# Kernel optimization log

Hardware: AMD Instinct MI355X
Metric: run time of the kernel (lower is better)

Reference implementation:

```python
import jax, jax.numpy as jnp
import numpy as np

B, S, D, H = 2, 2048, 1024, 16
DK = D // H  # 64


def setup_inputs() -> dict:
    key = jax.random.key(0)
    ks = jax.random.split(key, 11)
    scale = 1.0 / np.sqrt(D)
    inp = {
        "x": jax.random.normal(ks[0], (B, S, D), dtype=jnp.float32),
        "z": jax.random.normal(ks[1], (B, S, D), dtype=jnp.float32),
        # causal mask, broadcast over batch and heads; masked_fill where mask==0
        "mask": jnp.tril(jnp.ones((1, 1, S, S), dtype=jnp.int32)),
        "wq_w": jax.random.normal(ks[2], (D, D), dtype=jnp.float32) * scale,
        "wq_b": jax.random.normal(ks[3], (D,), dtype=jnp.float32) * 0.01,
        "wk_w": jax.random.normal(ks[4], (D, D), dtype=jnp.float32) * scale,
        "wk_b": jax.random.normal(ks[5], (D,), dtype=jnp.float32) * 0.01,
        "wv_w": jax.random.normal(ks[6], (D, D), dtype=jnp.float32) * scale,
        "wv_b": jax.random.normal(ks[7], (D,), dtype=jnp.float32) * 0.01,
        "wo_w": jax.random.normal(ks[8], (D, D), dtype=jnp.float32) * scale,
        "wo_b": jax.random.normal(ks[9], (D,), dtype=jnp.float32) * 0.01,
    }
    return inp


def reference(x, z, mask, wq_w, wq_b, wk_w, wk_b, wv_w, wv_b, wo_w, wo_b):
    # torch Linear: y = x @ W.T + b
    q = x @ wq_w.T + wq_b
    k = z @ wk_w.T + wk_b
    # NOTE: faithful to source bug: value uses wk, not wv (wv is a dead param)
    v = z @ wk_w.T + wk_b

    def split_heads(t):  # [B,S,D] -> [B,H,S,DK]
        return t.reshape(B, S, H, DK).transpose(0, 2, 1, 3)

    q, k, v = split_heads(q), split_heads(k), split_heads(v)

    scores = jnp.einsum("bhqd,bhkd->bhqk", q, k) * (DK ** -0.5)
    scores = jnp.where(mask == 0, -jnp.inf, scores)
    attn_weights = jax.nn.softmax(scores, axis=-1)  # [B,H,S,S]
    atn = jnp.einsum("bhqk,bhkd->bhqd", attn_weights, v)

    concat = atn.transpose(0, 2, 1, 3).reshape(B, S, D)
    output = concat @ wo_w.T + wo_b  # dropout rate 0.0 -> identity
    concat_attn_weight = attn_weights.sum(axis=1)  # [B,S,S]
    return output, concat_attn_weight
```

## Files before the change

### kernel.cpp

```cpp
#include <hip/hip_runtime.h>

typedef __bf16 bf16_t;
typedef __bf16 bf16x4 __attribute__((ext_vector_type(4)));
typedef __bf16 bf16x8 __attribute__((ext_vector_type(8)));
typedef float  f32x4  __attribute__((ext_vector_type(4)));

#define MFMA(a, b, c) __builtin_amdgcn_mfma_f32_16x16x32_bf16((a), (b), (c), 0, 0, 0)

static constexpr int Bsz = 2, S = 2048, D = 1024, H = 16, DK = 64;
#define QSCALE 0.18033688011112042f

__device__ __forceinline__ void gl16(const bf16_t* g, bf16_t* l)
{
    __builtin_amdgcn_global_load_lds(
        (const __attribute__((address_space(1))) void*)g,
        (__attribute__((address_space(3))) void*)l, 16, 0, 0);
}

__global__ __launch_bounds__(256) void cvt5(
    const float* __restrict__ x, const float* __restrict__ z,
    const float* __restrict__ wq, const float* __restrict__ wk,
    const float* __restrict__ wo,
    bf16_t* __restrict__ xb, bf16_t* __restrict__ zb,
    bf16_t* __restrict__ wqb, bf16_t* __restrict__ wkb, bf16_t* __restrict__ wob)
{
    constexpr int NXZ = Bsz * S * D / 4;
    constexpr int NW  = D * D / 4;
    int i = blockIdx.x * 256 + threadIdx.x;
    const float* s; bf16_t* d; int off;
    if (i < NXZ)                 { s = x;  d = xb;  off = i; }
    else if (i < 2 * NXZ)        { s = z;  d = zb;  off = i - NXZ; }
    else if (i < 2 * NXZ + NW)   { s = wq; d = wqb; off = i - 2 * NXZ; }
    else if (i < 2 * NXZ + 2*NW) { s = wk; d = wkb; off = i - 2 * NXZ - NW; }
    else                         { s = wo; d = wob; off = i - 2 * NXZ - 2 * NW; }
    float4 v = *(const float4*)&s[(size_t)off * 4];
    bf16x4 o;
    o[0] = (bf16_t)v.x; o[1] = (bf16_t)v.y; o[2] = (bf16_t)v.z; o[3] = (bf16_t)v.w;
    *(bf16x4*)&d[(size_t)off * 4] = o;
}

__global__ __launch_bounds__(512) void gemm_qk(
    const bf16_t* __restrict__ xA, const bf16_t* __restrict__ wqB,
    const float* __restrict__ wqb, bf16_t* __restrict__ Qc,
    const bf16_t* __restrict__ zA, const bf16_t* __restrict__ wkB,
    const float* __restrict__ wkb, bf16_t* __restrict__ Kc,
    bf16_t* __restrict__ KTout)
{
    constexpr int N = D, K = D;
    const int zi = blockIdx.z;
    const bf16_t* A    = zi ? zA  : xA;
    const bf16_t* B    = zi ? wkB : wqB;
    const float*  bias = zi ? wkb : wqb;
    bf16_t*       C    = zi ? Kc  : Qc;
    const float   sc   = zi ? 1.f : QSCALE;

    __shared__ bf16_t As[2][128][32];
    __shared__ bf16_t Bs[2][128][32];

    const int t    = threadIdx.x;
    const int wave = t >> 6, lane = t & 63;
    const int quad = lane >> 4, l15 = lane & 15;
    const int wm = (wave >> 1) * 32, wn = (wave & 1) * 64;
    const int rowbase = blockIdx.y * 128, colbase = blockIdx.x * 128;
    const int srow = wave * 16 + (lane >> 2);
    const int scol = (lane & 3) << 3;

    f32x4 acc[2][4];
#pragma unroll
    for (int i = 0; i < 2; ++i)
#pragma unroll
        for (int j = 0; j < 4; ++j) acc[i][j] = {0.f, 0.f, 0.f, 0.f};

    gl16(&A[(size_t)(rowbase + srow) * K + scol], &As[0][srow][scol]);
    gl16(&B[(size_t)(colbase + srow) * K + scol], &Bs[0][srow][scol]);
    __syncthreads();

    for (int kt = 0; kt < K; kt += 32) {
        const int cur = (kt >> 5) & 1, nxt = cur ^ 1;
        const bool more = (kt + 32) < K;
        if (more) {
            gl16(&A[(size_t)(rowbase + srow) * K + kt + 32 + scol], &As[nxt][srow][scol]);
            gl16(&B[(size_t)(colbase + srow) * K + kt + 32 + scol], &Bs[nxt][srow][scol]);
        }

        bf16x8 af[2], bfr[4];
#pragma unroll
        for (int mt = 0; mt < 2; ++mt)
            af[mt] = *(const bf16x8*)&As[cur][wm + mt * 16 + l15][quad * 8];
#pragma unroll
        for (int nt = 0; nt < 4; ++nt)
            bfr[nt] = *(const bf16x8*)&Bs[cur][wn + nt * 16 + l15][quad * 8];
#pragma unroll
        for (int mt = 0; mt < 2; ++mt)
#pragma unroll
            for (int nt = 0; nt < 4; ++nt)
                acc[mt][nt] = MFMA(af[mt], bfr[nt], acc[mt][nt]);

        __syncthreads();
    }

#pragma unroll
    for (int nt = 0; nt < 4; ++nt) {
        int col  = colbase + wn + nt * 16 + l15;
        float bv = bias[col];
#pragma unroll
        for (int mt = 0; mt < 2; ++mt) {
            int row0 = rowbase + wm + mt * 16 + quad * 4;
#pragma unroll
            for (int rr = 0; rr < 4; ++rr) {
                float v = (acc[mt][nt][rr] + bv) * sc;
                C[(size_t)(row0 + rr) * N + col] = (bf16_t)v;
                if (zi) {
                    int row = row0 + rr;
                    int bb = row >> 11, srw = row & (S - 1);
                    int hh = col >> 6,  dd  = col & 63;
                    KTout[(((size_t)bb * H + hh) * DK + dd) * S + srw] = (bf16_t)v;
                }
            }
        }
    }
}

__global__ __launch_bounds__(256) void gemm_obt(
    const bf16_t* __restrict__ A, const bf16_t* __restrict__ B,
    const float* __restrict__ bias, float* __restrict__ C)
{
    constexpr int N = D, K = D;
    __shared__ bf16_t As[2][64][32];
    __shared__ bf16_t Bs[2][128][32];

    const int t    = threadIdx.x;
    const int wave = t >> 6, lane = t & 63;
    const int quad = lane >> 4, l15 = lane & 15;
    const int wm = (wave >> 1) * 32, wn = (wave & 1) * 64;
    const int rowbase = blockIdx.y * 64, colbase = blockIdx.x * 128;
    const int srow = wave * 16 + (lane >> 2);
    const int scol = (lane & 3) << 3;

    f32x4 acc[2][4];
#pragma unroll
    for (int i = 0; i < 2; ++i)
#pragma unroll
        for (int j = 0; j < 4; ++j) acc[i][j] = {0.f, 0.f, 0.f, 0.f};

    gl16(&A[(size_t)(rowbase + srow) * K + scol],      &As[0][srow][scol]);
    gl16(&B[(size_t)(colbase + srow) * K + scol],      &Bs[0][srow][scol]);
    gl16(&B[(size_t)(colbase + 64 + srow) * K + scol], &Bs[0][64 + srow][scol]);
    __syncthreads();

    for (int kt = 0; kt < K; kt += 32) {
        const int cur = (kt >> 5) & 1, nxt = cur ^ 1;
        const bool more = (kt + 32) < K;
        if (more) {
            gl16(&A[(size_t)(rowbase + srow) * K + kt + 32 + scol],      &As[nxt][srow][scol]);
            gl16(&B[(size_t)(colbase + srow) * K + kt + 32 + scol],      &Bs[nxt][srow][scol]);
            gl16(&B[(size_t)(colbase + 64 + srow) * K + kt + 32 + scol], &Bs[nxt][64 + srow][scol]);
        }

        bf16x8 af[2], bfr[4];
#pragma unroll
        for (int mt = 0; mt < 2; ++mt)
            af[mt] = *(const bf16x8*)&As[cur][wm + mt * 16 + l15][quad * 8];
#pragma unroll
        for (int nt = 0; nt < 4; ++nt)
            bfr[nt] = *(const bf16x8*)&Bs[cur][wn + nt * 16 + l15][quad * 8];
#pragma unroll
        for (int mt = 0; mt < 2; ++mt)
#pragma unroll
            for (int nt = 0; nt < 4; ++nt)
                acc[mt][nt] = MFMA(af[mt], bfr[nt], acc[mt][nt]);

        __syncthreads();
    }

#pragma unroll
    for (int nt = 0; nt < 4; ++nt) {
        int col  = colbase + wn + nt * 16 + l15;
        float bv = bias[col];
#pragma unroll
        for (int mt = 0; mt < 2; ++mt) {
            int row0 = rowbase + wm + mt * 16 + quad * 4;
#pragma unroll
            for (int rr = 0; rr < 4; ++rr)
                C[(size_t)(row0 + rr) * N + col] = acc[mt][nt][rr] + bv;
        }
    }
}

__global__ __launch_bounds__(256) void attn_flash(
    const bf16_t* __restrict__ Q, const bf16_t* __restrict__ Km,
    const bf16_t* __restrict__ KT,
    bf16_t* __restrict__ Oc, float* __restrict__ m_ws, float* __restrict__ il_ws)
{
    const int h = blockIdx.y, b = blockIdx.z;
    const int t = threadIdx.x;
    const int wave = t >> 6, lane = t & 63;
    const int quad = lane >> 4, l15 = lane & 15;

    __shared__ bf16_t Ks[2][64][72];
    __shared__ bf16_t KTs[2][64][72];
    __shared__ bf16_t PQ[64][72];

    const int hcol = h * DK;
    const bf16_t* KTh = KT + ((size_t)(b * H + h)) * DK * S;
    const size_t bS = (size_t)b * S;

    const int jr = (t >> 3);
    const int ce = (t & 7) * 8;
    const int iloc = wave * 16 + l15;

    for (int half = 0; half < 2; ++half) {
        const int qt = half == 0 ? (int)blockIdx.x : 31 - (int)blockIdx.x;
        const size_t qrow0 = bS + (size_t)qt * 64;

        __syncthreads();
        bf16x8 qld[2], kreg[2], ktreg[2];
#pragma unroll
        for (int p = 0; p < 2; ++p) {
            qld[p]   = *(const bf16x8*)&Q[(qrow0 + p * 32 + jr) * D + hcol + ce];
            kreg[p]  = *(const bf16x8*)&Km[(bS + p * 32 + jr) * D + hcol + ce];
            ktreg[p] = *(const bf16x8*)&KTh[(size_t)(p * 32 + jr) * S + ce];
        }
#pragma unroll
        for (int p = 0; p < 2; ++p) {
            *(bf16x8*)&PQ[p * 32 + jr][ce]     = qld[p];
            *(bf16x8*)&Ks[0][p * 32 + jr][ce]  = kreg[p];
            *(bf16x8*)&KTs[0][p * 32 + jr][ce] = ktreg[p];
        }
        __syncthreads();
        const bf16x8 qf0 = *(const bf16x8*)&PQ[wave * 16 + l15][quad * 8];
        const bf16x8 qf1 = *(const bf16x8*)&PQ[wave * 16 + l15][32 + quad * 8];

        f32x4 accO[4];
#pragma unroll
        for (int u = 0; u < 4; ++u) accO[u] = {0.f, 0.f, 0.f, 0.f};
        float m_cur = -1e30f, l_cur = 0.f;

        auto softmax_pv = [&](f32x4 sv[4], int cur) {
            float tm = sv[0][0];
#pragma unroll
            for (int nt = 0; nt < 4; ++nt)
#pragma unroll
                for (int r = 0; r < 4; ++r) tm = fmaxf(tm, sv[nt][r]);
            tm = fmaxf(tm, __shfl_xor(tm, 16));
            tm = fmaxf(tm, __shfl_xor(tm, 32));
            if (__any(tm > m_cur + 8.f)) {
                float m_new = fmaxf(m_cur, tm);
                float alpha = exp2f(m_cur - m_new);
                m_cur = m_new;
                l_cur *= alpha;
                float alpha4[4];
#pragma unroll
                for (int r = 0; r < 4; ++r)
                    alpha4[r] = __shfl(alpha, (quad << 4) + quad * 4 + r, 64);
#pragma unroll
                for (int u = 0; u < 4; ++u)
#pragma unroll
                    for (int r = 0; r < 4; ++r) accO[u][r] *= alpha4[r];
            }
            float rs = 0.f;
#pragma unroll
            for (int nt = 0; nt < 4; ++nt)
#pragma unroll
                for (int r = 0; r < 4; ++r) {
                    float p = exp2f(sv[nt][r] - m_cur);
                    sv[nt][r] = p;
                    rs += p;
                }
            rs += __shfl_xor(rs, 16);
            rs += __shfl_xor(rs, 32);
            l_cur += rs;

#pragma unroll
            for (int nt = 0; nt < 4; ++nt) {
                bf16x4 pk;
                pk[0] = (bf16_t)sv[nt][0]; pk[1] = (bf16_t)sv[nt][1];
                pk[2] = (bf16_t)sv[nt][2]; pk[3] = (bf16_t)sv[nt][3];
                *(bf16x4*)&PQ[wave * 16 + l15][nt * 16 + quad * 4] = pk;
            }
            asm volatile("s_waitcnt lgkmcnt(0)" ::: "memory");

            bf16x8 pa0 = *(const bf16x8*)&PQ[wave * 16 + l15][quad * 8];
            bf16x8 pa1 = *(const bf16x8*)&PQ[wave * 16 + l15][32 + quad * 8];
            __builtin_amdgcn_s_setprio(1);
#pragma unroll
            for (int u = 0; u < 4; ++u) {
                bf16x8 v0 = *(const bf16x8*)&KTs[cur][u * 16 + l15][quad * 8];
                bf16x8 v1 = *(const bf16x8*)&KTs[cur][u * 16 + l15][32 + quad * 8];
                accO[u] = MFMA(pa0, v0, accO[u]);
                accO[u] = MFMA(pa1, v1, accO[u]);
            }
            __builtin_amdgcn_s_setprio(0);
        };

        for (int jt = 0; jt < qt; ++jt) {
            const int cur = jt & 1, nxt = cur ^ 1;
#pragma unroll
            for (int p = 0; p < 2; ++p) {
                kreg[p]  = *(const bf16x8*)&Km[(bS + (size_t)(jt + 1) * 64 + p * 32 + jr) * D + hcol + ce];
                ktreg[p] = *(const bf16x8*)&KTh[(size_t)(p * 32 + jr) * S + (size_t)(jt + 1) * 64 + ce];
            }

            f32x4 sv[4];
            __builtin_amdgcn_s_setprio(1);
#pragma unroll
            for (int nt = 0; nt < 4; ++nt) {
                bf16x8 a0 = *(const bf16x8*)&Ks[cur][nt * 16 + l15][quad * 8];
                bf16x8 a1 = *(const bf16x8*)&Ks[cur][nt * 16 + l15][32 + quad * 8];
                f32x4 a = {0.f, 0.f, 0.f, 0.f};
                a = MFMA(a0, qf0, a);
                a = MFMA(a1, qf1, a);
                sv[nt] = a;
            }
            __builtin_amdgcn_s_setprio(0);
            softmax_pv(sv, cur);

#pragma unroll
            for (int p = 0; p < 2; ++p) {
                *(bf16x8*)&Ks[nxt][p * 32 + jr][ce]  = kreg[p];
                *(bf16x8*)&KTs[nxt][p * 32 + jr][ce] = ktreg[p];
            }
            __syncthreads();
        }

        {
            const int cur = qt & 1;
            f32x4 sv[4];
            __builtin_amdgcn_s_setprio(1);
#pragma unroll
            for (int nt = 0; nt < 4; ++nt) {
                bf16x8 a0 = *(const bf16x8*)&Ks[cur][nt * 16 + l15][quad * 8];
                bf16x8 a1 = *(const bf16x8*)&Ks[cur][nt * 16 + l15][32 + quad * 8];
                f32x4 a = {0.f, 0.f, 0.f, 0.f};
                a = MFMA(a0, qf0, a);
                a = MFMA(a1, qf1, a);
#pragma unroll
                for (int r = 0; r < 4; ++r)
                    if ((nt * 16 + quad * 4 + r) > iloc) a[r] = -1e30f;
                sv[nt] = a;
            }
            __builtin_amdgcn_s_setprio(0);
            softmax_pv(sv, cur);
        }

        float invl = 1.f / l_cur;
        float invl4[4];
#pragma unroll
        for (int r = 0; r < 4; ++r)
            invl4[r] = __shfl(invl, (quad << 4) + quad * 4 + r, 64);
#pragma unroll
        for (int u = 0; u < 4; ++u)
#pragma unroll
            for (int r = 0; r < 4; ++r)
                Oc[(qrow0 + wave * 16 + quad * 4 + r) * D + hcol + u * 16 + l15] =
                    (bf16_t)(accO[u][r] * invl4[r]);

        if (quad == 0) {
            size_t sb = ((size_t)(b * H + h)) * S + (size_t)qt * 64 + wave * 16 + l15;
            m_ws[sb]  = m_cur;
            il_ws[sb] = invl;
        }
    }
}

__global__ __launch_bounds__(256) void attn_wsum(
    const bf16_t* __restrict__ Q, const bf16_t* __restrict__ Km,
    const float* __restrict__ m_ws, const float* __restrict__ il_ws,
    float* __restrict__ out2)
{
    const int jt = blockIdx.x, qt = blockIdx.y, b = blockIdx.z;
    const int t  = threadIdx.x;
    float* tile = out2 + (size_t)b * S * S + (size_t)qt * 64 * S + (size_t)jt * 64;

    if (jt > qt) {
        int r0 = t >> 2, c0 = (t & 3) * 16;
#pragma unroll
        for (int e = 0; e < 16; ++e) tile[(size_t)r0 * S + c0 + e] = 0.f;
        return;
    }

    const int wave = t >> 6, lane = t & 63;
    const int quad = lane >> 4, l15 = lane & 15;
    __shared__ bf16_t Ks[2][64][72];
    __shared__ bf16_t Qs[2][64][72];

    const int jr = (t >> 3), ce = (t & 7) * 8;
    const size_t krow = (size_t)b * S + (size_t)jt * 64;
    const size_t qrow = (size_t)b * S + (size_t)qt * 64;

    f32x4 accs[4];
#pragma unroll
    for (int nt = 0; nt < 4; ++nt) accs[nt] = {0.f, 0.f, 0.f, 0.f};

    bf16x8 kreg[2], qreg[2];
#pragma unroll
    for (int p = 0; p < 2; ++p) {
        kreg[p] = *(const bf16x8*)&Km[(krow + p * 32 + jr) * D + ce];
        qreg[p] = *(const bf16x8*)&Q[(qrow + p * 32 + jr) * D + ce];
    }
#pragma unroll
    for (int p = 0; p < 2; ++p) {
        *(bf16x8*)&Ks[0][p * 32 + jr][ce] = kreg[p];
        *(bf16x8*)&Qs[0][p * 32 + jr][ce] = qreg[p];
    }
    __syncthreads();

    const size_t mlb0 = (size_t)(b * H) * S + (size_t)qt * 64 + wave * 16 + quad * 4;

    if (jt < qt) {
        for (int h = 0; h < H; ++h) {
            const int cur = h & 1, nxt = cur ^ 1;
            if (h < H - 1) {
                const int hc = (h + 1) * DK;
#pragma unroll
                for (int p = 0; p < 2; ++p) {
                    kreg[p] = *(const bf16x8*)&Km[(krow + p * 32 + jr) * D + hc + ce];
                    qreg[p] = *(const bf16x8*)&Q[(qrow + p * 32 + jr) * D + hc + ce];
                }
            }

            bf16x8 qf0 = *(const bf16x8*)&Qs[cur][wave * 16 + l15][quad * 8];
            bf16x8 qf1 = *(const bf16x8*)&Qs[cur][wave * 16 + l15][32 + quad * 8];
            f32x4 mr = *(const f32x4*)&m_ws[mlb0 + (size_t)h * S];
            f32x4 il = *(const f32x4*)&il_ws[mlb0 + (size_t)h * S];

#pragma unroll
            for (int nt = 0; nt < 4; ++nt) {
                bf16x8 k0 = *(const bf16x8*)&Ks[cur][nt * 16 + l15][quad * 8];
                bf16x8 k1 = *(const bf16x8*)&Ks[cur][nt * 16 + l15][32 + quad * 8];
                f32x4 a = {0.f, 0.f, 0.f, 0.f};
                a = MFMA(qf0, k0, a);
                a = MFMA(qf1, k1, a);
#pragma unroll
                for (int r = 0; r < 4; ++r)
                    accs[nt][r] = fmaf(exp2f(a[r] - mr[r]), il[r], accs[nt][r]);
            }

            if (h < H - 1) {
#pragma unroll
                for (int p = 0; p < 2; ++p) {
                    *(bf16x8*)&Ks[nxt][p * 32 + jr][ce] = kreg[p];
                    *(bf16x8*)&Qs[nxt][p * 32 + jr][ce] = qreg[p];
                }
            }
            __syncthreads();
        }
    } else {
        for (int h = 0; h < H; ++h) {
            const int cur = h & 1, nxt = cur ^ 1;
            if (h < H - 1) {
                const int hc = (h + 1) * DK;
#pragma unroll
                for (int p = 0; p < 2; ++p) {
                    kreg[p] = *(const bf16x8*)&Km[(krow + p * 32 + jr) * D + hc + ce];
                    qreg[p] = *(const bf16x8*)&Q[(qrow + p * 32 + jr) * D + hc + ce];
                }
            }

            bf16x8 qf0 = *(const bf16x8*)&Qs[cur][wave * 16 + l15][quad * 8];
            bf16x8 qf1 = *(const bf16x8*)&Qs[cur][wave * 16 + l15][32 + quad * 8];
            f32x4 mr = *(const f32x4*)&m_ws[mlb0 + (size_t)h * S];
            f32x4 il = *(const f32x4*)&il_ws[mlb0 + (size_t)h * S];

#pragma unroll
            for (int nt = 0; nt < 4; ++nt) {
                bf16x8 k0 = *(const bf16x8*)&Ks[cur][nt * 16 + l15][quad * 8];
                bf16x8 k1 = *(const bf16x8*)&Ks[cur][nt * 16 + l15][32 + quad * 8];
                f32x4 a = {0.f, 0.f, 0.f, 0.f};
                a = MFMA(qf0, k0, a);
                a = MFMA(qf1, k1, a);
#pragma unroll
                for (int r = 0; r < 4; ++r) {
                    int i = wave * 16 + quad * 4 + r;
                    int j = nt * 16 + l15;
                    float p = (j <= i) ? exp2f(a[r] - mr[r]) * il[r] : 0.f;
                    accs[nt][r] += p;
                }
            }

            if (h < H - 1) {
#pragma unroll
                for (int p = 0; p < 2; ++p) {
                    *(bf16x8*)&Ks[nxt][p * 32 + jr][ce] = kreg[p];
                    *(bf16x8*)&Qs[nxt][p * 32 + jr][ce] = qreg[p];
                }
            }
            __syncthreads();
        }
    }

#pragma unroll
    for (int nt = 0; nt < 4; ++nt)
#pragma unroll
        for (int r = 0; r < 4; ++r)
            tile[(size_t)(wave * 16 + quad * 4 + r) * S + nt * 16 + l15] = accs[nt][r];
}

extern "C" void kernel_launch(void* const* d_in, const int* in_sizes, int n_in,
                              void* d_out, int out_size, void* d_ws, size_t ws_size,
                              hipStream_t stream)
{
    const float* x    = (const float*)d_in[0];
    const float* z    = (const float*)d_in[1];
    const float* wq_w = (const float*)d_in[3];
    const float* wq_b = (const float*)d_in[4];
    const float* wk_w = (const float*)d_in[5];
    const float* wk_b = (const float*)d_in[6];
    const float* wo_w = (const float*)d_in[9];
    const float* wo_b = (const float*)d_in[10];

    float* out  = (float*)d_out;
    float* out2 = out + (size_t)Bsz * S * D;

    float*  m_ws  = (float*)d_ws;
    float*  il_ws = m_ws + (size_t)Bsz * H * S;
    bf16_t* Qws   = (bf16_t*)(il_ws + (size_t)Bsz * H * S);
    bf16_t* Kws   = Qws + (size_t)Bsz * S * D;
    bf16_t* wq_bf = Kws + (size_t)Bsz * S * D;
    bf16_t* wk_bf = wq_bf + (size_t)D * D;
    bf16_t* wo_bf = wk_bf + (size_t)D * D;
    bf16_t* xb    = (bf16_t*)out;
    bf16_t* zb    = xb + (size_t)Bsz * S * D;
    bf16_t* Cc    = (bf16_t*)out2;
    bf16_t* KTws  = Cc + (size_t)Bsz * S * D;

    constexpr int CVT_BLOCKS = (2 * (Bsz * S * D / 4) + 3 * (D * D / 4)) / 256;
    cvt5<<<dim3(CVT_BLOCKS), dim3(256), 0, stream>>>(
        x, z, wq_w, wk_w, wo_w, xb, zb, wq_bf, wk_bf, wo_bf);
    gemm_qk<<<dim3(D / 128, (Bsz * S) / 128, 2), dim3(512), 0, stream>>>(
        xb, wq_bf, wq_b, Qws, zb, wk_bf, wk_b, Kws, KTws);
    attn_flash<<<dim3(S / 128, H, Bsz), dim3(256), 0, stream>>>(
        Qws, Kws, KTws, Cc, m_ws, il_ws);
    gemm_obt<<<dim3(D / 128, (Bsz * S) / 64, 1), dim3(256), 0, stream>>>(
        Cc, wo_bf, wo_b, out);
    attn_wsum<<<dim3(S / 64, S / 64, Bsz), dim3(256), 0, stream>>>(
        Qws, Kws, m_ws, il_ws, out2);
}
```

Measured before the change: 271.8 us.

## Process both paired query tiles concurrently in one 512-thread block sharing K/V tiles

The flash-attention kernel previously processed two query tiles (qt and 31-qt) sequentially within a 256-thread block, reloading K/V tiles for each. Now the block runs 8 waves, with two groups of 4 waves each handling one query tile, and streams K/V tiles once up to the larger tile index, so both groups share the same LDS loads. This halves K/V global traffic and doubles the waves per block for more latency hiding. The cost is that the group with the smaller tile sits idle at the barriers for the remaining iterations, and the larger block raises register and LDS pressure per CU.

```diff
diff --git a/kernel.cpp b/kernel.cpp
--- a/kernel.cpp
+++ b/kernel.cpp
@@ -187,7 +187,7 @@
     }
 }
 
-__global__ __launch_bounds__(256) void attn_flash(
+__global__ __launch_bounds__(512) void attn_flash(
     const bf16_t* __restrict__ Q, const bf16_t* __restrict__ Km,
     const bf16_t* __restrict__ KT,
     bf16_t* __restrict__ Oc, float* __restrict__ m_ws, float* __restrict__ il_ws)
@@ -196,111 +196,113 @@
     const int t = threadIdx.x;
     const int wave = t >> 6, lane = t & 63;
     const int quad = lane >> 4, l15 = lane & 15;
+    const int grp  = wave >> 2;
+    const int wl   = wave & 3;
 
     __shared__ bf16_t Ks[2][64][72];
     __shared__ bf16_t KTs[2][64][72];
-    __shared__ bf16_t PQ[64][72];
+    __shared__ bf16_t PQ[128][72];
 
     const int hcol = h * DK;
     const bf16_t* KTh = KT + ((size_t)(b * H + h)) * DK * S;
     const size_t bS = (size_t)b * S;
 
-    const int jr = (t >> 3);
+    const int jr = t >> 3;
     const int ce = (t & 7) * 8;
-    const int iloc = wave * 16 + l15;
-
-    for (int half = 0; half < 2; ++half) {
-        const int qt = half == 0 ? (int)blockIdx.x : 31 - (int)blockIdx.x;
-        const size_t qrow0 = bS + (size_t)qt * 64;
-
-        __syncthreads();
-        bf16x8 qld[2], kreg[2], ktreg[2];
-#pragma unroll
-        for (int p = 0; p < 2; ++p) {
-            qld[p]   = *(const bf16x8*)&Q[(qrow0 + p * 32 + jr) * D + hcol + ce];
-            kreg[p]  = *(const bf16x8*)&Km[(bS + p * 32 + jr) * D + hcol + ce];
-            ktreg[p] = *(const bf16x8*)&KTh[(size_t)(p * 32 + jr) * S + ce];
-        }
-#pragma unroll
-        for (int p = 0; p < 2; ++p) {
-            *(bf16x8*)&PQ[p * 32 + jr][ce]     = qld[p];
-            *(bf16x8*)&Ks[0][p * 32 + jr][ce]  = kreg[p];
-            *(bf16x8*)&KTs[0][p * 32 + jr][ce] = ktreg[p];
-        }
-        __syncthreads();
-        const bf16x8 qf0 = *(const bf16x8*)&PQ[wave * 16 + l15][quad * 8];
-        const bf16x8 qf1 = *(const bf16x8*)&PQ[wave * 16 + l15][32 + quad * 8];
-
-        f32x4 accO[4];
-#pragma unroll
-        for (int u = 0; u < 4; ++u) accO[u] = {0.f, 0.f, 0.f, 0.f};
-        float m_cur = -1e30f, l_cur = 0.f;
-
-        auto softmax_pv = [&](f32x4 sv[4], int cur) {
-            float tm = sv[0][0];
-#pragma unroll
-            for (int nt = 0; nt < 4; ++nt)
-#pragma unroll
-                for (int r = 0; r < 4; ++r) tm = fmaxf(tm, sv[nt][r]);
-            tm = fmaxf(tm, __shfl_xor(tm, 16));
-            tm = fmaxf(tm, __shfl_xor(tm, 32));
-            if (__any(tm > m_cur + 8.f)) {
-                float m_new = fmaxf(m_cur, tm);
-                float alpha = exp2f(m_cur - m_new);
-                m_cur = m_new;
-                l_cur *= alpha;
-                float alpha4[4];
-#pragma unroll
-                for (int r = 0; r < 4; ++r)
-                    alpha4[r] = __shfl(alpha, (quad << 4) + quad * 4 + r, 64);
-#pragma unroll
-                for (int u = 0; u < 4; ++u)
-#pragma unroll
-                    for (int r = 0; r < 4; ++r) accO[u][r] *= alpha4[r];
-            }
-            float rs = 0.f;
-#pragma unroll
-            for (int nt = 0; nt < 4; ++nt)
-#pragma unroll
-                for (int r = 0; r < 4; ++r) {
-                    float p = exp2f(sv[nt][r] - m_cur);
-                    sv[nt][r] = p;
-                    rs += p;
-                }
-            rs += __shfl_xor(rs, 16);
-            rs += __shfl_xor(rs, 32);
-            l_cur += rs;
-
-#pragma unroll
-            for (int nt = 0; nt < 4; ++nt) {
-                bf16x4 pk;
-                pk[0] = (bf16_t)sv[nt][0]; pk[1] = (bf16_t)sv[nt][1];
-                pk[2] = (bf16_t)sv[nt][2]; pk[3] = (bf16_t)sv[nt][3];
-                *(bf16x4*)&PQ[wave * 16 + l15][nt * 16 + quad * 4] = pk;
-            }
-            asm volatile("s_waitcnt lgkmcnt(0)" ::: "memory");
-
-            bf16x8 pa0 = *(const bf16x8*)&PQ[wave * 16 + l15][quad * 8];
-            bf16x8 pa1 = *(const bf16x8*)&PQ[wave * 16 + l15][32 + quad * 8];
-            __builtin_amdgcn_s_setprio(1);
-#pragma unroll
-            for (int u = 0; u < 4; ++u) {
-                bf16x8 v0 = *(const bf16x8*)&KTs[cur][u * 16 + l15][quad * 8];
-                bf16x8 v1 = *(const bf16x8*)&KTs[cur][u * 16 + l15][32 + quad * 8];
-                accO[u] = MFMA(pa0, v0, accO[u]);
-                accO[u] = MFMA(pa1, v1, accO[u]);
-            }
-            __builtin_amdgcn_s_setprio(0);
-        };
-
-        for (int jt = 0; jt < qt; ++jt) {
-            const int cur = jt & 1, nxt = cur ^ 1;
-#pragma unroll
-            for (int p = 0; p < 2; ++p) {
-                kreg[p]  = *(const bf16x8*)&Km[(bS + (size_t)(jt + 1) * 64 + p * 32 + jr) * D + hcol + ce];
-                ktreg[p] = *(const bf16x8*)&KTh[(size_t)(p * 32 + jr) * S + (size_t)(jt + 1) * 64 + ce];
-            }
-
+    const int iloc = wl * 16 + l15;
+    const int prow = grp * 64 + wl * 16 + l15;
+
+    const int qtA = (int)blockIdx.x;
+    const int qtB = 31 - qtA;
+    const int qt  = grp ? qtB : qtA;
+    const size_t qrow0 = bS + (size_t)qt * 64;
+
+    {
+        bf16x8 qa  = *(const bf16x8*)&Q[(bS + (size_t)qtA * 64 + jr) * D + hcol + ce];
+        bf16x8 qb  = *(const bf16x8*)&Q[(bS + (size_t)qtB * 64 + jr) * D + hcol + ce];
+        bf16x8 k0  = *(const bf16x8*)&Km[(bS + jr) * D + hcol + ce];
+        bf16x8 kt0 = *(const bf16x8*)&KTh[(size_t)jr * S + ce];
+        *(bf16x8*)&PQ[jr][ce]      = qa;
+        *(bf16x8*)&PQ[64 + jr][ce] = qb;
+        *(bf16x8*)&Ks[0][jr][ce]   = k0;
+        *(bf16x8*)&KTs[0][jr][ce]  = kt0;
+    }
+    __syncthreads();
+    const bf16x8 qf0 = *(const bf16x8*)&PQ[prow][quad * 8];
+    const bf16x8 qf1 = *(const bf16x8*)&PQ[prow][32 + quad * 8];
+
+    f32x4 accO[4];
+#pragma unroll
+    for (int u = 0; u < 4; ++u) accO[u] = {0.f, 0.f, 0.f, 0.f};
+    float m_cur = -1e30f, l_cur = 0.f;
+
+    auto softmax_pv = [&](f32x4 sv[4], int cur) {
+        float tm = sv[0][0];
+#pragma unroll
+        for (int nt = 0; nt < 4; ++nt)
+#pragma unroll
+            for (int r = 0; r < 4; ++r) tm = fmaxf(tm, sv[nt][r]);
+        tm = fmaxf(tm, __shfl_xor(tm, 16));
+        tm = fmaxf(tm, __shfl_xor(tm, 32));
+        if (__any(tm > m_cur + 8.f)) {
+            float m_new = fmaxf(m_cur, tm);
+            float alpha = exp2f(m_cur - m_new);
+            m_cur = m_new;
+            l_cur *= alpha;
+            float alpha4[4];
+#pragma unroll
+            for (int r = 0; r < 4; ++r)
+                alpha4[r] = __shfl(alpha, (quad << 4) + quad * 4 + r, 64);
+#pragma unroll
+            for (int u = 0; u < 4; ++u)
+#pragma unroll
+                for (int r = 0; r < 4; ++r) accO[u][r] *= alpha4[r];
+        }
+        float rs = 0.f;
+#pragma unroll
+        for (int nt = 0; nt < 4; ++nt)
+#pragma unroll
+            for (int r = 0; r < 4; ++r) {
+                float p = exp2f(sv[nt][r] - m_cur);
+                sv[nt][r] = p;
+                rs += p;
+            }
+        rs += __shfl_xor(rs, 16);
+        rs += __shfl_xor(rs, 32);
+        l_cur += rs;
+
+#pragma unroll
+        for (int nt = 0; nt < 4; ++nt) {
+            bf16x4 pk;
+            pk[0] = (bf16_t)sv[nt][0]; pk[1] = (bf16_t)sv[nt][1];
+            pk[2] = (bf16_t)sv[nt][2]; pk[3] = (bf16_t)sv[nt][3];
+            *(bf16x4*)&PQ[prow][nt * 16 + quad * 4] = pk;
+        }
+        asm volatile("s_waitcnt lgkmcnt(0)" ::: "memory");
+
+        bf16x8 pa0 = *(const bf16x8*)&PQ[prow][quad * 8];
+        bf16x8 pa1 = *(const bf16x8*)&PQ[prow][32 + quad * 8];
+        __builtin_amdgcn_s_setprio(1);
+#pragma unroll
+        for (int u = 0; u < 4; ++u) {
+            bf16x8 v0 = *(const bf16x8*)&KTs[cur][u * 16 + l15][quad * 8];
+            bf16x8 v1 = *(const bf16x8*)&KTs[cur][u * 16 + l15][32 + quad * 8];
+            accO[u] = MFMA(pa0, v0, accO[u]);
+            accO[u] = MFMA(pa1, v1, accO[u]);
+        }
+        __builtin_amdgcn_s_setprio(0);
+    };
+
+    for (int jt = 0; jt <= qtB; ++jt) {
+        const int cur = jt & 1, nxt = cur ^ 1;
+        const bool more = jt < qtB;
+        bf16x8 kreg, ktreg;
+        if (more) {
+            kreg  = *(const bf16x8*)&Km[(bS + (size_t)(jt + 1) * 64 + jr) * D + hcol + ce];
+            ktreg = *(const bf16x8*)&KTh[(size_t)jr * S + (size_t)(jt + 1) * 64 + ce];
+        }
+
+        if (jt <= qt) {
             f32x4 sv[4];
             __builtin_amdgcn_s_setprio(1);
 #pragma unroll
@@ -313,53 +315,39 @@
                 sv[nt] = a;
             }
             __builtin_amdgcn_s_setprio(0);
+            if (jt == qt) {
+#pragma unroll
+                for (int nt = 0; nt < 4; ++nt)
+#pragma unroll
+                    for (int r = 0; r < 4; ++r)
+                        if ((nt * 16 + quad * 4 + r) > iloc) sv[nt][r] = -1e30f;
+            }
             softmax_pv(sv, cur);
-
-#pragma unroll
-            for (int p = 0; p < 2; ++p) {
-                *(bf16x8*)&Ks[nxt][p * 32 + jr][ce]  = kreg[p];
-                *(bf16x8*)&KTs[nxt][p * 32 + jr][ce] = ktreg[p];
-            }
-            __syncthreads();
-        }
-
-        {
-            const int cur = qt & 1;
-            f32x4 sv[4];
-            __builtin_amdgcn_s_setprio(1);
-#pragma unroll
-            for (int nt = 0; nt < 4; ++nt) {
-                bf16x8 a0 = *(const bf16x8*)&Ks[cur][nt * 16 + l15][quad * 8];
-                bf16x8 a1 = *(const bf16x8*)&Ks[cur][nt * 16 + l15][32 + quad * 8];
-                f32x4 a = {0.f, 0.f, 0.f, 0.f};
-                a = MFMA(a0, qf0, a);
-                a = MFMA(a1, qf1, a);
-#pragma unroll
-                for (int r = 0; r < 4; ++r)
-                    if ((nt * 16 + quad * 4 + r) > iloc) a[r] = -1e30f;
-                sv[nt] = a;
-            }
-            __builtin_amdgcn_s_setprio(0);
-            softmax_pv(sv, cur);
-        }
-
-        float invl = 1.f / l_cur;
-        float invl4[4];
+        }
+
+        if (more) {
+            *(bf16x8*)&Ks[nxt][jr][ce]  = kreg;
+            *(bf16x8*)&KTs[nxt][jr][ce] = ktreg;
+        }
+        __syncthreads();
+    }
+
+    float invl = 1.f / l_cur;
+    float invl4[4];
+#pragma unroll
+    for (int r = 0; r < 4; ++r)
+        invl4[r] = __shfl(invl, (quad << 4) + quad * 4 + r, 64);
+#pragma unroll
+    for (int u = 0; u < 4; ++u)
 #pragma unroll
         for (int r = 0; r < 4; ++r)
-            invl4[r] = __shfl(invl, (quad << 4) + quad * 4 + r, 64);
-#pragma unroll
-        for (int u = 0; u < 4; ++u)
-#pragma unroll
-            for (int r = 0; r < 4; ++r)
-                Oc[(qrow0 + wave * 16 + quad * 4 + r) * D + hcol + u * 16 + l15] =
-                    (bf16_t)(accO[u][r] * invl4[r]);
-
-        if (quad == 0) {
-            size_t sb = ((size_t)(b * H + h)) * S + (size_t)qt * 64 + wave * 16 + l15;
-            m_ws[sb]  = m_cur;
-            il_ws[sb] = invl;
-        }
+            Oc[(qrow0 + wl * 16 + quad * 4 + r) * D + hcol + u * 16 + l15] =
+                (bf16_t)(accO[u][r] * invl4[r]);
+
+    if (quad == 0) {
+        size_t sb = ((size_t)(b * H + h)) * S + (size_t)qt * 64 + wl * 16 + l15;
+        m_ws[sb]  = m_cur;
+        il_ws[sb] = invl;
     }
 }
 
@@ -529,7 +517,7 @@
         x, z, wq_w, wk_w, wo_w, xb, zb, wq_bf, wk_bf, wo_bf);
     gemm_qk<<<dim3(D / 128, (Bsz * S) / 128, 2), dim3(512), 0, stream>>>(
         xb, wq_bf, wq_b, Qws, zb, wk_bf, wk_b, Kws, KTws);
-    attn_flash<<<dim3(S / 128, H, Bsz), dim3(256), 0, stream>>>(
+    attn_flash<<<dim3(S / 128, H, Bsz), dim3(512), 0, stream>>>(
         Qws, Kws, KTws, Cc, m_ws, il_ws);
     gemm_obt<<<dim3(D / 128, (Bsz * S) / 64, 1), dim3(256), 0, stream>>>(
         Cc, wo_bf, wo_b, out);
```

Result: no change. 269.4 us (-0.9%).
